# Performance work log

Hardware: AMD Instinct MI355X
Metric: run time of the kernel (lower is better)

The kernel has to match this reference:

```python
import jax, jax.numpy as jnp
from jax import lax
import numpy as np

B, N, C = 128, 196, 768
H = 8
HD = C // H  # 96
FF = 3       # focusing factor
KS = 5       # dwc kernel size


def setup_inputs() -> dict:
    key = jax.random.key(0)
    ks = jax.random.split(key, 12)
    std = 0.02
    inp = {
        'x': jax.random.normal(ks[0], (B, N, C), dtype=jnp.float32),
        'Wq': jax.random.normal(ks[1], (C, C), dtype=jnp.float32) * std,
        'bq': jnp.zeros((C,), dtype=jnp.float32),
        'Wk': jax.random.normal(ks[2], (C, C), dtype=jnp.float32) * std,
        'bk': jnp.zeros((C,), dtype=jnp.float32),
        'Wv': jax.random.normal(ks[3], (C, C), dtype=jnp.float32) * std,
        'bv': jnp.zeros((C,), dtype=jnp.float32),
        'pos_enc': jax.random.normal(ks[4], (1, N, C), dtype=jnp.float32) * std,
        'scale_param': jnp.zeros((1, 1, C), dtype=jnp.float32),
        'dwc_w': jax.random.normal(ks[5], (HD, 1, KS, KS), dtype=jnp.float32) * np.sqrt(2.0 / (KS * KS)),
        'dwc_b': jnp.zeros((HD,), dtype=jnp.float32),
        'Wp': jax.random.normal(ks[6], (C, C), dtype=jnp.float32) * std,
        'bp': jnp.zeros((C,), dtype=jnp.float32),
    }
    return inp


def _focused_attn(x, Wq, bq, Wk, bk, Wv, bv, pos_enc, scale_param, dwc_w, dwc_b, Wp, bp):
    b, n, c = x.shape
    q = x @ Wq + bq
    k = x @ Wk + bk
    v = x @ Wv + bv
    k = k + pos_enc

    scale = jax.nn.softplus(scale_param)
    q = (jax.nn.relu(q) + 1e-6) / scale
    k = (jax.nn.relu(k) + 1e-6) / scale
    # focusing: raise to power FF, restore original L2 norm (over full channel dim)
    q_norm = jnp.linalg.norm(q, axis=-1, keepdims=True)
    k_norm = jnp.linalg.norm(k, axis=-1, keepdims=True)
    q = q ** FF
    k = k ** FF
    q = q / jnp.linalg.norm(q, axis=-1, keepdims=True) * q_norm
    k = k / jnp.linalg.norm(k, axis=-1, keepdims=True) * k_norm

    # (b, n, H*hd) -> (b*H, n, hd)
    def split_heads(t):
        return t.reshape(b, n, H, HD).transpose(0, 2, 1, 3).reshape(b * H, n, HD)

    q, k, v = split_heads(q), split_heads(k), split_heads(v)

    i = j = n
    cdim = ddim = HD
    z = 1.0 / (jnp.einsum('bic,bc->bi', q, k.sum(axis=1)) + 1e-6)
    if i * j * (cdim + ddim) > cdim * ddim * (i + j):
        kv = jnp.einsum('bjc,bjd->bcd', k, v)              # (b*H, hd, hd)
        out = jnp.einsum('bic,bcd,bi->bid', q, kv, z)
    else:
        qk = jnp.einsum('bic,bjc->bij', q, k)
        out = jnp.einsum('bij,bjd,bi->bid', qk, v, z)

    # depthwise conv feature map on v reshaped to sqrt(n) x sqrt(n)
    num = int(round(n ** 0.5))
    fm = v.transpose(0, 2, 1).reshape(b * H, HD, num, num)
    fm = lax.conv_general_dilated(
        fm, dwc_w, window_strides=(1, 1), padding='SAME',
        feature_group_count=HD,
        dimension_numbers=('NCHW', 'OIHW', 'NCHW'))
    fm = fm + dwc_b[None, :, None, None]
    fm = fm.reshape(b * H, HD, n).transpose(0, 2, 1)

    out = out + fm
    out = out.reshape(b, H, n, HD).transpose(0, 2, 1, 3).reshape(b, n, c)
    return out @ Wp + bp


def reference(x, Wq, bq, Wk, bk, Wv, bv, pos_enc, scale_param, dwc_w, dwc_b, Wp, bp):
    return _focused_attn(x, Wq, bq, Wk, bk, Wv, bv, pos_enc, scale_param, dwc_w, dwc_b, Wp, bp)
```

## Files before the change

### kernel.cpp

```cpp
#include <hip/hip_runtime.h>
#include <hip/hip_bf16.h>
#include <math.h>


#define MROWS 25088
#define CDIM 768
#define HDIM 96
#define NTOK 196
#define BHN 1024
#define K2 1536

typedef __attribute__((ext_vector_type(8))) short bf16x8;
typedef __attribute__((ext_vector_type(4))) float f32x4;

__device__ __forceinline__ short f2bf(float x) {
  unsigned u = __float_as_uint(x);
  unsigned r = (u + 0x7fffu + ((u >> 16) & 1u)) >> 16;
  return (short)r;
}
__device__ __forceinline__ float bf2f(short s) {
  return __uint_as_float(((unsigned)(unsigned short)s) << 16);
}

__device__ __forceinline__ void gload16(const short* g, short* l) {
  __builtin_amdgcn_global_load_lds(
      (const __attribute__((address_space(1))) void*)g,
      (__attribute__((address_space(3))) void*)l, 16, 0, 0);
}

__device__ __forceinline__ unsigned cvt2(float x, float y, float& rx, float& ry) {
  __hip_bfloat162 hb = __float22bfloat162_rn(make_float2(x, y));
  float2 hf = __bfloat1622float2(hb);
  rx = x - hf.x; ry = y - hf.y;
  unsigned u;
  __builtin_memcpy(&u, &hb, 4);
  return u;
}
__device__ __forceinline__ unsigned cvt2n(float x, float y) {
  __hip_bfloat162 hb = __float22bfloat162_rn(make_float2(x, y));
  unsigned u;
  __builtin_memcpy(&u, &hb, 4);
  return u;
}

__global__ __launch_bounds__(256) void split_wt(const float* __restrict__ W0,
                                                const float* __restrict__ W1,
                                                const float* __restrict__ W2,
                                                const float* __restrict__ W3,
                                                short* __restrict__ outbase) {
  const float* W;
  switch (blockIdx.z) {
    case 0: W = W0; break;
    case 1: W = W1; break;
    case 2: W = W2; break;
    default: W = W3; break;
  }
  short* O = outbase + (size_t)blockIdx.z * 768 * K2;
  __shared__ float t[32][33];
  const int n0 = blockIdx.x * 32, k0 = blockIdx.y * 32;
  const int tx = threadIdx.x & 31, ty = threadIdx.x >> 5;
#pragma unroll
  for (int i = 0; i < 32; i += 8) t[ty + i][tx] = W[(size_t)(k0 + ty + i) * 768 + n0 + tx];
  __syncthreads();
#pragma unroll
  for (int i = 0; i < 32; i += 8) {
    float v = t[tx][ty + i];
    short h = f2bf(v), l = f2bf(v - bf2f(h));
    O[(size_t)(n0 + ty + i) * K2 + k0 + tx] = h;
    O[(size_t)(n0 + ty + i) * K2 + 768 + k0 + tx] = l;
  }
}

__device__ __forceinline__ void gemm_mfma_body(const float* __restrict__ A,
                                               const short* __restrict__ Bt2,
                                               const float* __restrict__ bias,
                                               const float* __restrict__ pos,
                                               float* __restrict__ C, bool addPos) {
  __shared__ short Ah[128 * 32];
  __shared__ short Al[128 * 32];
  __shared__ short Bh[128 * 32];
  __shared__ short Bl[128 * 32];
  const int tid = threadIdx.x;
  const int lane = tid & 63;
  const int w = tid >> 6, wr = w >> 1, wc = w & 1;

  const int hw = blockIdx.x + 6 * blockIdx.y;
  const int tile = (hw & 7) * 147 + (hw >> 3);
  const int bx = tile % 6, by = tile / 6;
  const int row0 = by * 128, col0 = bx * 128;

  const int ar = tid >> 1;
  const int ah_ = tid & 1;
  const int am = (tid >> 2) & 3;
  const int s0 = (2 * ah_) ^ am, s1 = (2 * ah_ + 1) ^ am;
  const float* gA = A + (size_t)(row0 + ar) * CDIM + ah_ * 16;
  short* lAh0 = Ah + ar * 32 + s0 * 8;
  short* lAh1 = Ah + ar * 32 + s1 * 8;
  short* lAl0 = Al + ar * 32 + s0 * 8;
  short* lAl1 = Al + ar * 32 + s1 * 8;

  const int brow = w * 32 + (lane >> 2);
  const int bslot = (lane & 3) ^ ((lane >> 3) & 3);
  const short* gBh = Bt2 + (size_t)(col0 + brow) * K2 + bslot * 8;
  const short* gBl = gBh + 768;
  short* ldsBh0 = Bh + (w * 32) * 32;
  short* ldsBh1 = Bh + (w * 32 + 16) * 32;
  short* ldsBl0 = Bl + (w * 32) * 32;
  short* ldsBl1 = Bl + (w * 32 + 16) * 32;

  f32x4 acc[4][4];
#pragma unroll
  for (int i = 0; i < 4; i++)
#pragma unroll
    for (int j = 0; j < 4; j++) acc[i][j] = (f32x4){0.f, 0.f, 0.f, 0.f};

  const int fr = lane & 15;
  const int k16 = lane >> 4;
  const int rslot = k16 ^ ((fr >> 1) & 3);
  const int rofs = fr * 32 + rslot * 8;

#pragma unroll 1
  for (int k0 = 0; k0 < CDIM; k0 += 32) {
    float4 a0 = *(const float4*)(gA + k0);
    float4 a1 = *(const float4*)(gA + k0 + 4);
    float4 a2 = *(const float4*)(gA + k0 + 8);
    float4 a3 = *(const float4*)(gA + k0 + 12);
    float r[16];
    unsigned h0 = cvt2(a0.x, a0.y, r[0], r[1]);
    unsigned h1 = cvt2(a0.z, a0.w, r[2], r[3]);
    unsigned h2 = cvt2(a1.x, a1.y, r[4], r[5]);
    unsigned h3 = cvt2(a1.z, a1.w, r[6], r[7]);
    unsigned h4 = cvt2(a2.x, a2.y, r[8], r[9]);
    unsigned h5 = cvt2(a2.z, a2.w, r[10], r[11]);
    unsigned h6 = cvt2(a3.x, a3.y, r[12], r[13]);
    unsigned h7 = cvt2(a3.z, a3.w, r[14], r[15]);
    unsigned l0 = cvt2n(r[0], r[1]),  l1 = cvt2n(r[2], r[3]);
    unsigned l2 = cvt2n(r[4], r[5]),  l3 = cvt2n(r[6], r[7]);
    unsigned l4 = cvt2n(r[8], r[9]),  l5 = cvt2n(r[10], r[11]);
    unsigned l6 = cvt2n(r[12], r[13]), l7 = cvt2n(r[14], r[15]);

    __syncthreads();
    gload16(gBh + k0, ldsBh0);
    gload16(gBh + 16 * K2 + k0, ldsBh1);
    gload16(gBl + k0, ldsBl0);
    gload16(gBl + 16 * K2 + k0, ldsBl1);
    *(uint4*)lAh0 = make_uint4(h0, h1, h2, h3);
    *(uint4*)lAh1 = make_uint4(h4, h5, h6, h7);
    *(uint4*)lAl0 = make_uint4(l0, l1, l2, l3);
    *(uint4*)lAl1 = make_uint4(l4, l5, l6, l7);
    __syncthreads();

    bf16x8 fah[4], fal[4], fbh[4], fbl[4];
#pragma unroll
    for (int i = 0; i < 4; i++) {
      const int arr = (wr * 64 + i * 16) * 32 + rofs;
      const int brr = (wc * 64 + i * 16) * 32 + rofs;
      fah[i] = *(const bf16x8*)&Ah[arr];
      fal[i] = *(const bf16x8*)&Al[arr];
      fbh[i] = *(const bf16x8*)&Bh[brr];
      fbl[i] = *(const bf16x8*)&Bl[brr];
    }
#pragma unroll
    for (int i = 0; i < 4; i++)
#pragma unroll
      for (int j = 0; j < 4; j++)
        acc[i][j] = __builtin_amdgcn_mfma_f32_16x16x32_bf16(fah[i], fbh[j], acc[i][j], 0, 0, 0);
#pragma unroll
    for (int i = 0; i < 4; i++)
#pragma unroll
      for (int j = 0; j < 4; j++)
        acc[i][j] = __builtin_amdgcn_mfma_f32_16x16x32_bf16(fah[i], fbl[j], acc[i][j], 0, 0, 0);
#pragma unroll
    for (int i = 0; i < 4; i++)
#pragma unroll
      for (int j = 0; j < 4; j++)
        acc[i][j] = __builtin_amdgcn_mfma_f32_16x16x32_bf16(fal[i], fbh[j], acc[i][j], 0, 0, 0);
  }

  const int rg = (lane >> 4) * 4;
#pragma unroll
  for (int i = 0; i < 4; i++) {
#pragma unroll
    for (int j = 0; j < 4; j++) {
      f32x4 v = acc[i][j];
      const int gcol = col0 + wc * 64 + j * 16 + fr;
      const float bb = bias[gcol];
#pragma unroll
      for (int r2 = 0; r2 < 4; r2++) {
        const int grow = row0 + wr * 64 + i * 16 + rg + r2;
        float val = v[r2] + bb;
        if (addPos) val += pos[(grow % NTOK) * CDIM + gcol];
        C[(size_t)grow * CDIM + gcol] = val;
      }
    }
  }
}

__global__ __launch_bounds__(256) void mfma_qkv(const float* __restrict__ x,
    const short* __restrict__ wt2,
    const float* __restrict__ b0, const float* __restrict__ b1, const float* __restrict__ b2,
    const float* __restrict__ pos,
    float* __restrict__ o0, float* __restrict__ o1, float* __restrict__ o2) {
  const short* Bt; const float* bias; float* C; bool addPos = false;
  switch (blockIdx.z) {
    case 0: Bt = wt2;                         bias = b0; C = o0; break;
    case 1: Bt = wt2 + (size_t)768 * K2;      bias = b1; C = o1; addPos = true; break;
    default: Bt = wt2 + (size_t)2 * 768 * K2; bias = b2; C = o2; break;
  }
  gemm_mfma_body(x, Bt, bias, pos, C, addPos);
}

__global__ __launch_bounds__(256) void mfma_proj(const float* __restrict__ y,
    const short* __restrict__ wt2p, const float* __restrict__ bias,
    float* __restrict__ C) {
  gemm_mfma_body(y, wt2p, bias, nullptr, C, false);
}

__device__ __forceinline__ void wave_reduce2(float& a, float& b) {
#pragma unroll
  for (int off = 32; off > 0; off >>= 1) {
    a += __shfl_xor(a, off, 64);
    b += __shfl_xor(b, off, 64);
  }
}

__global__ __launch_bounds__(256) void focus_kernel(float* __restrict__ q,
                                                    float* __restrict__ k,
                                                    const float* __restrict__ sp) {
  const int row = blockIdx.x * 4 + (threadIdx.x >> 6);
  const int lane = threadIdx.x & 63;
  float* qb = q + (size_t)row * CDIM;
  float* kb = k + (size_t)row * CDIM;

  float tq[12], tk[12];
  float sq = 0.f, sk = 0.f;
#pragma unroll
  for (int s = 0; s < 3; s++) {
    const int c = s * 256 + lane * 4;
    float4 qv = *(const float4*)&qb[c];
    float4 kv4 = *(const float4*)&kb[c];
    float4 spv = *(const float4*)&sp[c];
#pragma unroll
    for (int j = 0; j < 4; j++) {
      float scp = j == 0 ? spv.x : j == 1 ? spv.y : j == 2 ? spv.z : spv.w;
      float qq  = j == 0 ? qv.x  : j == 1 ? qv.y  : j == 2 ? qv.z  : qv.w;
      float kk  = j == 0 ? kv4.x : j == 1 ? kv4.y : j == 2 ? kv4.z : kv4.w;
      float scale = fmaxf(scp, 0.f) + log1pf(expf(-fabsf(scp)));
      float inv = 1.f / scale;
      float aq = (fmaxf(qq, 0.f) + 1e-6f) * inv;
      float ak = (fmaxf(kk, 0.f) + 1e-6f) * inv;
      tq[s * 4 + j] = aq; tk[s * 4 + j] = ak;
      sq += aq * aq; sk += ak * ak;
    }
  }
  wave_reduce2(sq, sk);
  const float nq1 = sqrtf(sq), nk1 = sqrtf(sk);

  float s2q = 0.f, s2k = 0.f;
#pragma unroll
  for (int j = 0; j < 12; j++) {
    float cq = tq[j] * tq[j] * tq[j];
    float ck = tk[j] * tk[j] * tk[j];
    s2q += cq * cq; s2k += ck * ck;
  }
  wave_reduce2(s2q, s2k);
  const float rq = nq1 / sqrtf(s2q);
  const float rk = nk1 / sqrtf(s2k);

#pragma unroll
  for (int s = 0; s < 3; s++) {
    const int c = s * 256 + lane * 4;
    float4 oq, ok;
#pragma unroll
    for (int j = 0; j < 4; j++) {
      float a = tq[s * 4 + j], b = tk[s * 4 + j];
      float vq = a * a * a * rq, vk = b * b * b * rk;
      if (j == 0) { oq.x = vq; ok.x = vk; }
      else if (j == 1) { oq.y = vq; ok.y = vk; }
      else if (j == 2) { oq.z = vq; ok.z = vk; }
      else { oq.w = vq; ok.w = vk; }
    }
    *(float4*)&qb[c] = oq;
    *(float4*)&kb[c] = ok;
  }
}

__global__ __launch_bounds__(128) void ksum_kernel(const float* __restrict__ k,
                                                   float* __restrict__ ksum) {
  const int bh = blockIdx.x;
  const int b = bh >> 3, h = bh & 7;
  const int d = threadIdx.x;
  if (d >= HDIM) return;
  const float* base = k + (size_t)(b * NTOK) * CDIM + h * HDIM + d;
  float s = 0.f;
  for (int j = 0; j < NTOK; ++j) s += base[(size_t)j * CDIM];
  ksum[bh * HDIM + d] = s;
}

__global__ __launch_bounds__(256) void kv_kernel(const float* __restrict__ k,
                                                 const float* __restrict__ v,
                                                 float* __restrict__ kv) {
  const int bh = blockIdx.x;
  const int b = bh >> 3, h = bh & 7;
  const size_t base = (size_t)(b * NTOK) * CDIM + h * HDIM;
  __shared__ float ks[28][96];
  __shared__ float vs[28][96];
  const int tid = threadIdx.x;
  const int tx = tid & 15, ty = tid >> 4;
  float acc[6][6];
#pragma unroll
  for (int i = 0; i < 6; i++)
#pragma unroll
    for (int j = 0; j < 6; j++) acc[i][j] = 0.f;

  for (int j0 = 0; j0 < NTOK; j0 += 28) {
    for (int idx = tid; idx < 28 * 96; idx += 256) {
      int jr = idx / 96, d = idx % 96;
      size_t g = base + (size_t)(j0 + jr) * CDIM + d;
      ks[jr][d] = k[g];
      vs[jr][d] = v[g];
    }
    __syncthreads();
#pragma unroll 4
    for (int j = 0; j < 28; ++j) {
      float a[6], bb[6];
#pragma unroll
      for (int i = 0; i < 6; i++) a[i] = ks[j][ty * 6 + i];
#pragma unroll
      for (int i = 0; i < 6; i++) bb[i] = vs[j][tx * 6 + i];
#pragma unroll
      for (int i = 0; i < 6; i++)
#pragma unroll
        for (int jj = 0; jj < 6; jj++) acc[i][jj] += a[i] * bb[jj];
    }
    __syncthreads();
  }
#pragma unroll
  for (int i = 0; i < 6; i++)
#pragma unroll
    for (int j = 0; j < 6; j++)
      kv[(size_t)bh * (HDIM * HDIM) + (ty * 6 + i) * HDIM + tx * 6 + j] = acc[i][j];
}

__global__ __launch_bounds__(256) void attn_out_kernel(const float* __restrict__ q,
                                                       const float* __restrict__ kvmat,
                                                       const float* __restrict__ ksum,
                                                       float* __restrict__ y) {
  const int bh = blockIdx.x;
  const int b = bh >> 3, h = bh & 7;
  const size_t base = (size_t)(b * NTOK) * CDIM + h * HDIM;
  __shared__ float kvs[HDIM * HDIM];
  __shared__ float qs[64][97];
  __shared__ float ksum_s[HDIM];
  const int tid = threadIdx.x;
  const int tx = tid & 15, ty = tid >> 4;
  const int d0 = tx * 6;

  for (int idx = tid; idx < HDIM * HDIM; idx += 256) kvs[idx] = kvmat[(size_t)bh * (HDIM * HDIM) + idx];
  if (tid < HDIM) ksum_s[tid] = ksum[bh * HDIM + tid];

  for (int i0 = 0; i0 < NTOK; i0 += 64) {
    int nrows = NTOK - i0; if (nrows > 64) nrows = 64;
    __syncthreads();
    for (int idx = tid; idx < nrows * 96; idx += 256) {
      int rr = idx / 96, d = idx % 96;
      qs[rr][d] = q[base + (size_t)(i0 + rr) * CDIM + d];
    }
    __syncthreads();

    float zz[4];
#pragma unroll
    for (int rr = 0; rr < 4; rr++) {
      int r2 = ty * 4 + rr;
      float part = 0.f;
#pragma unroll
      for (int i = 0; i < 6; i++) part += qs[r2][d0 + i] * ksum_s[d0 + i];
#pragma unroll
      for (int m = 8; m >= 1; m >>= 1) part += __shfl_xor(part, m, 16);
      zz[rr] = 1.f / (part + 1e-6f);
    }

    float acc[4][6];
#pragma unroll
    for (int rr = 0; rr < 4; rr++)
#pragma unroll
      for (int i = 0; i < 6; i++) acc[rr][i] = 0.f;

    for (int c = 0; c < HDIM; ++c) {
      float kvv[6];
#pragma unroll
      for (int i = 0; i < 6; i++) kvv[i] = kvs[c * HDIM + d0 + i];
#pragma unroll
      for (int rr = 0; rr < 4; rr++) {
        float qv = qs[ty * 4 + rr][c];
#pragma unroll
        for (int i = 0; i < 6; i++) acc[rr][i] += qv * kvv[i];
      }
    }
#pragma unroll
    for (int rr = 0; rr < 4; rr++) {
      int r2 = i0 + ty * 4 + rr;
      if (r2 < NTOK) {
#pragma unroll
        for (int i = 0; i < 6; i++) y[base + (size_t)r2 * CDIM + d0 + i] = acc[rr][i] * zz[rr];
      }
    }
  }
}

__global__ __launch_bounds__(256) void dwconv_kernel(const float* __restrict__ v,
                                                     const float* __restrict__ w,
                                                     const float* __restrict__ bias,
                                                     float* __restrict__ y) {
  const int bh = blockIdx.x;
  const int b = bh >> 3, h = bh & 7;
  const int ch0 = blockIdx.y * 32;
  const size_t base = (size_t)(b * NTOK) * CDIM + h * HDIM + ch0;
  __shared__ float vs[NTOK][32];
  __shared__ float ws_s[32][25];
  const int tid = threadIdx.x;

  for (int idx = tid; idx < NTOK * 32; idx += 256) {
    int j = idx >> 5, ch = idx & 31;
    vs[j][ch] = v[base + (size_t)j * CDIM + ch];
  }
  for (int idx = tid; idx < 32 * 25; idx += 256) {
    int ch = idx / 25, kk = idx % 25;
    ws_s[ch][kk] = w[(ch0 + ch) * 25 + kk];
  }
  __syncthreads();

  const int ch = tid & 31, pg = tid >> 5;
  const float bval = bias[ch0 + ch];
  for (int p = pg; p < NTOK; p += 8) {
    int r2 = p / 14, cl = p % 14;
    float acc = 0.f;
#pragma unroll
    for (int dr = 0; dr < 5; dr++) {
      int rr = r2 + dr - 2;
      if (rr < 0 || rr >= 14) continue;
#pragma unroll
      for (int dc = 0; dc < 5; dc++) {
        int cc = cl + dc - 2;
        if (cc < 0 || cc >= 14) continue;
        acc += vs[rr * 14 + cc][ch] * ws_s[ch][dr * 5 + dc];
      }
    }
    y[base + (size_t)p * CDIM + ch] += acc + bval;
  }
}

extern "C" void kernel_launch(void* const* d_in, const int* in_sizes, int n_in,
                              void* d_out, int out_size, void* d_ws, size_t ws_size,
                              hipStream_t stream) {
  const float* x    = (const float*)d_in[0];
  const float* Wq   = (const float*)d_in[1];
  const float* bq   = (const float*)d_in[2];
  const float* Wk   = (const float*)d_in[3];
  const float* bk   = (const float*)d_in[4];
  const float* Wv   = (const float*)d_in[5];
  const float* bv   = (const float*)d_in[6];
  const float* pos  = (const float*)d_in[7];
  const float* sp   = (const float*)d_in[8];
  const float* dwcw = (const float*)d_in[9];
  const float* dwcb = (const float*)d_in[10];
  const float* Wp   = (const float*)d_in[11];
  const float* bp   = (const float*)d_in[12];
  float* out = (float*)d_out;

  const size_t MC = (size_t)MROWS * CDIM;
  char* ws = (char*)d_ws;
  float* k    = (float*)(ws);
  float* v    = (float*)(ws + MC * 4);
  short* wt2  = (short*)(ws + 2 * MC * 4);
  float* kv   = (float*)(ws + 2 * MC * 4 + (size_t)4 * 768 * K2 * 2);
  float* ksum = kv + (size_t)BHN * HDIM * HDIM;
  float* q = out;
  float* y = k;

  split_wt<<<dim3(24, 24, 4), 256, 0, stream>>>(Wq, Wk, Wv, Wp, wt2);
  mfma_qkv<<<dim3(6, 196, 3), 256, 0, stream>>>(x, wt2, bq, bk, bv, pos, q, k, v);
  focus_kernel<<<MROWS / 4, 256, 0, stream>>>(q, k, sp);
  ksum_kernel<<<BHN, 128, 0, stream>>>(k, ksum);
  kv_kernel<<<BHN, 256, 0, stream>>>(k, v, kv);
  attn_out_kernel<<<BHN, 256, 0, stream>>>(q, kv, ksum, y);
  dwconv_kernel<<<dim3(BHN, 3), 256, 0, stream>>>(v, dwcw, dwcb, y);
  mfma_proj<<<dim3(6, 196, 1), 256, 0, stream>>>(y, wt2 + (size_t)3 * 768 * K2, bp, out);
}
```

Measured before the change: 937.6 us.

## Pre-split activations into bf16 hi/lo and load GEMM A tiles via direct LDS

Adds a split_act kernel that converts x into bf16 hi/lo pairs once, and has dwconv write the projection input y directly in split form. Both GEMMs then load A and B with global_load_lds instead of converting fp32 A inside the k-loop. ksum is folded into kv_kernel, and some LDS reads are vectorized. This trades extra global write/read passes for the split activations against removing the repeated per-block conversion work and register pressure in the GEMM loops.

```diff
diff --git a/kernel.cpp b/kernel.cpp
--- a/kernel.cpp
+++ b/kernel.cpp
@@ -26,21 +26,6 @@
   __builtin_amdgcn_global_load_lds(
       (const __attribute__((address_space(1))) void*)g,
       (__attribute__((address_space(3))) void*)l, 16, 0, 0);
-}
-
-__device__ __forceinline__ unsigned cvt2(float x, float y, float& rx, float& ry) {
-  __hip_bfloat162 hb = __float22bfloat162_rn(make_float2(x, y));
-  float2 hf = __bfloat1622float2(hb);
-  rx = x - hf.x; ry = y - hf.y;
-  unsigned u;
-  __builtin_memcpy(&u, &hb, 4);
-  return u;
-}
-__device__ __forceinline__ unsigned cvt2n(float x, float y) {
-  __hip_bfloat162 hb = __float22bfloat162_rn(make_float2(x, y));
-  unsigned u;
-  __builtin_memcpy(&u, &hb, 4);
-  return u;
 }
 
 __global__ __launch_bounds__(256) void split_wt(const float* __restrict__ W0,
@@ -71,11 +56,26 @@
   }
 }
 
-__device__ __forceinline__ void gemm_mfma_body(const float* __restrict__ A,
-                                               const short* __restrict__ Bt2,
-                                               const float* __restrict__ bias,
-                                               const float* __restrict__ pos,
-                                               float* __restrict__ C, bool addPos) {
+__global__ __launch_bounds__(256) void split_act(const float* __restrict__ in,
+                                                 short* __restrict__ out2) {
+  int idx = blockIdx.x * 256 + threadIdx.x;
+  if (idx >= MROWS * 192) return;
+  int m = idx / 192, c4 = (idx % 192) * 4;
+  float4 v = *(const float4*)&in[(size_t)m * CDIM + c4];
+  short4 hi, lo;
+  hi.x = f2bf(v.x); lo.x = f2bf(v.x - bf2f(hi.x));
+  hi.y = f2bf(v.y); lo.y = f2bf(v.y - bf2f(hi.y));
+  hi.z = f2bf(v.z); lo.z = f2bf(v.z - bf2f(hi.z));
+  hi.w = f2bf(v.w); lo.w = f2bf(v.w - bf2f(hi.w));
+  *(short4*)&out2[(size_t)m * K2 + c4] = hi;
+  *(short4*)&out2[(size_t)m * K2 + 768 + c4] = lo;
+}
+
+__device__ __forceinline__ void gemm_mfma_body_pre(const short* __restrict__ A2,
+                                                   const short* __restrict__ Bt2,
+                                                   const float* __restrict__ bias,
+                                                   const float* __restrict__ pos,
+                                                   float* __restrict__ C, bool addPos) {
   __shared__ short Ah[128 * 32];
   __shared__ short Al[128 * 32];
   __shared__ short Bh[128 * 32];
@@ -89,24 +89,18 @@
   const int bx = tile % 6, by = tile / 6;
   const int row0 = by * 128, col0 = bx * 128;
 
-  const int ar = tid >> 1;
-  const int ah_ = tid & 1;
-  const int am = (tid >> 2) & 3;
-  const int s0 = (2 * ah_) ^ am, s1 = (2 * ah_ + 1) ^ am;
-  const float* gA = A + (size_t)(row0 + ar) * CDIM + ah_ * 16;
-  short* lAh0 = Ah + ar * 32 + s0 * 8;
-  short* lAh1 = Ah + ar * 32 + s1 * 8;
-  short* lAl0 = Al + ar * 32 + s0 * 8;
-  short* lAl1 = Al + ar * 32 + s1 * 8;
-
-  const int brow = w * 32 + (lane >> 2);
-  const int bslot = (lane & 3) ^ ((lane >> 3) & 3);
-  const short* gBh = Bt2 + (size_t)(col0 + brow) * K2 + bslot * 8;
-  const short* gBl = gBh + 768;
-  short* ldsBh0 = Bh + (w * 32) * 32;
-  short* ldsBh1 = Bh + (w * 32 + 16) * 32;
-  short* ldsBl0 = Bl + (w * 32) * 32;
-  short* ldsBl1 = Bl + (w * 32 + 16) * 32;
+  const int srow = w * 32 + (lane >> 2);
+  const int slot = (lane & 3) ^ ((lane >> 3) & 3);
+  const short* gA = A2 + (size_t)(row0 + srow) * K2 + slot * 8;
+  const short* gB = Bt2 + (size_t)(col0 + srow) * K2 + slot * 8;
+  short* dA0 = Ah + (w * 32) * 32;
+  short* dA1 = Ah + (w * 32 + 16) * 32;
+  short* dAl0 = Al + (w * 32) * 32;
+  short* dAl1 = Al + (w * 32 + 16) * 32;
+  short* dB0 = Bh + (w * 32) * 32;
+  short* dB1 = Bh + (w * 32 + 16) * 32;
+  short* dBl0 = Bl + (w * 32) * 32;
+  short* dBl1 = Bl + (w * 32 + 16) * 32;
 
   f32x4 acc[4][4];
 #pragma unroll
@@ -121,33 +115,15 @@
 
 #pragma unroll 1
   for (int k0 = 0; k0 < CDIM; k0 += 32) {
-    float4 a0 = *(const float4*)(gA + k0);
-    float4 a1 = *(const float4*)(gA + k0 + 4);
-    float4 a2 = *(const float4*)(gA + k0 + 8);
-    float4 a3 = *(const float4*)(gA + k0 + 12);
-    float r[16];
-    unsigned h0 = cvt2(a0.x, a0.y, r[0], r[1]);
-    unsigned h1 = cvt2(a0.z, a0.w, r[2], r[3]);
-    unsigned h2 = cvt2(a1.x, a1.y, r[4], r[5]);
-    unsigned h3 = cvt2(a1.z, a1.w, r[6], r[7]);
-    unsigned h4 = cvt2(a2.x, a2.y, r[8], r[9]);
-    unsigned h5 = cvt2(a2.z, a2.w, r[10], r[11]);
-    unsigned h6 = cvt2(a3.x, a3.y, r[12], r[13]);
-    unsigned h7 = cvt2(a3.z, a3.w, r[14], r[15]);
-    unsigned l0 = cvt2n(r[0], r[1]),  l1 = cvt2n(r[2], r[3]);
-    unsigned l2 = cvt2n(r[4], r[5]),  l3 = cvt2n(r[6], r[7]);
-    unsigned l4 = cvt2n(r[8], r[9]),  l5 = cvt2n(r[10], r[11]);
-    unsigned l6 = cvt2n(r[12], r[13]), l7 = cvt2n(r[14], r[15]);
-
-    __syncthreads();
-    gload16(gBh + k0, ldsBh0);
-    gload16(gBh + 16 * K2 + k0, ldsBh1);
-    gload16(gBl + k0, ldsBl0);
-    gload16(gBl + 16 * K2 + k0, ldsBl1);
-    *(uint4*)lAh0 = make_uint4(h0, h1, h2, h3);
-    *(uint4*)lAh1 = make_uint4(h4, h5, h6, h7);
-    *(uint4*)lAl0 = make_uint4(l0, l1, l2, l3);
-    *(uint4*)lAl1 = make_uint4(l4, l5, l6, l7);
+    __syncthreads();
+    gload16(gA + k0, dA0);
+    gload16(gA + 16 * K2 + k0, dA1);
+    gload16(gA + 768 + k0, dAl0);
+    gload16(gA + 768 + 16 * K2 + k0, dAl1);
+    gload16(gB + k0, dB0);
+    gload16(gB + 16 * K2 + k0, dB1);
+    gload16(gB + 768 + k0, dBl0);
+    gload16(gB + 768 + 16 * K2 + k0, dBl1);
     __syncthreads();
 
     bf16x8 fah[4], fal[4], fbh[4], fbl[4];
@@ -196,7 +172,7 @@
   }
 }
 
-__global__ __launch_bounds__(256) void mfma_qkv(const float* __restrict__ x,
+__global__ __launch_bounds__(256) void mfma_qkv_pre(const short* __restrict__ x2,
     const short* __restrict__ wt2,
     const float* __restrict__ b0, const float* __restrict__ b1, const float* __restrict__ b2,
     const float* __restrict__ pos,
@@ -207,13 +183,13 @@
     case 1: Bt = wt2 + (size_t)768 * K2;      bias = b1; C = o1; addPos = true; break;
     default: Bt = wt2 + (size_t)2 * 768 * K2; bias = b2; C = o2; break;
   }
-  gemm_mfma_body(x, Bt, bias, pos, C, addPos);
-}
-
-__global__ __launch_bounds__(256) void mfma_proj(const float* __restrict__ y,
+  gemm_mfma_body_pre(x2, Bt, bias, pos, C, addPos);
+}
+
+__global__ __launch_bounds__(256) void mfma_proj_pre(const short* __restrict__ y2,
     const short* __restrict__ wt2p, const float* __restrict__ bias,
     float* __restrict__ C) {
-  gemm_mfma_body(y, wt2p, bias, nullptr, C, false);
+  gemm_mfma_body_pre(y2, wt2p, bias, nullptr, C, false);
 }
 
 __device__ __forceinline__ void wave_reduce2(float& a, float& b) {
@@ -285,21 +261,10 @@
   }
 }
 
-__global__ __launch_bounds__(128) void ksum_kernel(const float* __restrict__ k,
-                                                   float* __restrict__ ksum) {
-  const int bh = blockIdx.x;
-  const int b = bh >> 3, h = bh & 7;
-  const int d = threadIdx.x;
-  if (d >= HDIM) return;
-  const float* base = k + (size_t)(b * NTOK) * CDIM + h * HDIM + d;
-  float s = 0.f;
-  for (int j = 0; j < NTOK; ++j) s += base[(size_t)j * CDIM];
-  ksum[bh * HDIM + d] = s;
-}
-
 __global__ __launch_bounds__(256) void kv_kernel(const float* __restrict__ k,
                                                  const float* __restrict__ v,
-                                                 float* __restrict__ kv) {
+                                                 float* __restrict__ kv,
+                                                 float* __restrict__ ksum) {
   const int bh = blockIdx.x;
   const int b = bh >> 3, h = bh & 7;
   const size_t base = (size_t)(b * NTOK) * CDIM + h * HDIM;
@@ -312,6 +277,7 @@
   for (int i = 0; i < 6; i++)
 #pragma unroll
     for (int j = 0; j < 6; j++) acc[i][j] = 0.f;
+  float kcol = 0.f;
 
   for (int j0 = 0; j0 < NTOK; j0 += 28) {
     for (int idx = tid; idx < 28 * 96; idx += 256) {
@@ -321,13 +287,17 @@
       vs[jr][d] = v[g];
     }
     __syncthreads();
+    if (tid < 96) {
+#pragma unroll
+      for (int jr = 0; jr < 28; ++jr) kcol += ks[jr][tid];
+    }
 #pragma unroll 4
     for (int j = 0; j < 28; ++j) {
       float a[6], bb[6];
 #pragma unroll
-      for (int i = 0; i < 6; i++) a[i] = ks[j][ty * 6 + i];
-#pragma unroll
-      for (int i = 0; i < 6; i++) bb[i] = vs[j][tx * 6 + i];
+      for (int i = 0; i < 3; i++) *(float2*)&a[i * 2]  = *(const float2*)&ks[j][ty * 6 + i * 2];
+#pragma unroll
+      for (int i = 0; i < 3; i++) *(float2*)&bb[i * 2] = *(const float2*)&vs[j][tx * 6 + i * 2];
 #pragma unroll
       for (int i = 0; i < 6; i++)
 #pragma unroll
@@ -340,6 +310,7 @@
 #pragma unroll
     for (int j = 0; j < 6; j++)
       kv[(size_t)bh * (HDIM * HDIM) + (ty * 6 + i) * HDIM + tx * 6 + j] = acc[i][j];
+  if (tid < 96) ksum[bh * HDIM + tid] = kcol;
 }
 
 __global__ __launch_bounds__(256) void attn_out_kernel(const float* __restrict__ q,
@@ -389,7 +360,7 @@
     for (int c = 0; c < HDIM; ++c) {
       float kvv[6];
 #pragma unroll
-      for (int i = 0; i < 6; i++) kvv[i] = kvs[c * HDIM + d0 + i];
+      for (int i = 0; i < 3; i++) *(float2*)&kvv[i * 2] = *(const float2*)&kvs[c * HDIM + d0 + i * 2];
 #pragma unroll
       for (int rr = 0; rr < 4; rr++) {
         float qv = qs[ty * 4 + rr][c];
@@ -411,11 +382,13 @@
 __global__ __launch_bounds__(256) void dwconv_kernel(const float* __restrict__ v,
                                                      const float* __restrict__ w,
                                                      const float* __restrict__ bias,
-                                                     float* __restrict__ y) {
+                                                     const float* __restrict__ y,
+                                                     short* __restrict__ y2) {
   const int bh = blockIdx.x;
   const int b = bh >> 3, h = bh & 7;
   const int ch0 = blockIdx.y * 32;
   const size_t base = (size_t)(b * NTOK) * CDIM + h * HDIM + ch0;
+  const size_t col = h * HDIM + ch0;
   __shared__ float vs[NTOK][32];
   __shared__ float ws_s[32][25];
   const int tid = threadIdx.x;
@@ -446,7 +419,12 @@
         acc += vs[rr * 14 + cc][ch] * ws_s[ch][dr * 5 + dc];
       }
     }
-    y[base + (size_t)p * CDIM + ch] += acc + bval;
+    float val = y[base + (size_t)p * CDIM + ch] + acc + bval;
+    short hh = f2bf(val);
+    short ll = f2bf(val - bf2f(hh));
+    const size_t row = (size_t)(b * NTOK + p);
+    y2[row * K2 + col + ch] = hh;
+    y2[row * K2 + 768 + col + ch] = ll;
   }
 }
 
@@ -469,21 +447,25 @@
   float* out = (float*)d_out;
 
   const size_t MC = (size_t)MROWS * CDIM;
+  const size_t WT2B = (size_t)4 * 768 * K2 * 2;
   char* ws = (char*)d_ws;
   float* k    = (float*)(ws);
   float* v    = (float*)(ws + MC * 4);
   short* wt2  = (short*)(ws + 2 * MC * 4);
-  float* kv   = (float*)(ws + 2 * MC * 4 + (size_t)4 * 768 * K2 * 2);
-  float* ksum = kv + (size_t)BHN * HDIM * HDIM;
+  char* R3 = ws + 2 * MC * 4 + WT2B;
+  short* x2   = (short*)R3;
+  float* kv   = (float*)R3;
+  float* ksum = (float*)(R3 + (size_t)BHN * HDIM * HDIM * 4);
+  short* y2   = (short*)R3;
   float* q = out;
   float* y = k;
 
   split_wt<<<dim3(24, 24, 4), 256, 0, stream>>>(Wq, Wk, Wv, Wp, wt2);
-  mfma_qkv<<<dim3(6, 196, 3), 256, 0, stream>>>(x, wt2, bq, bk, bv, pos, q, k, v);
+  split_act<<<(MROWS * 192 + 255) / 256, 256, 0, stream>>>(x, x2);
+  mfma_qkv_pre<<<dim3(6, 196, 3), 256, 0, stream>>>(x2, wt2, bq, bk, bv, pos, q, k, v);
   focus_kernel<<<MROWS / 4, 256, 0, stream>>>(q, k, sp);
-  ksum_kernel<<<BHN, 128, 0, stream>>>(k, ksum);
-  kv_kernel<<<BHN, 256, 0, stream>>>(k, v, kv);
+  kv_kernel<<<BHN, 256, 0, stream>>>(k, v, kv, ksum);
   attn_out_kernel<<<BHN, 256, 0, stream>>>(q, kv, ksum, y);
-  dwconv_kernel<<<dim3(BHN, 3), 256, 0, stream>>>(v, dwcw, dwcb, y);
-  mfma_proj<<<dim3(6, 196, 1), 256, 0, stream>>>(y, wt2 + (size_t)3 * 768 * K2, bp, out);
-}
+  dwconv_kernel<<<dim3(BHN, 3), 256, 0, stream>>>(v, dwcw, dwcb, y, y2);
+  mfma_proj_pre<<<dim3(6, 196, 1), 256, 0, stream>>>(y2, wt2 + (size_t)3 * 768 * K2, bp, out);
+}
```

Result: no change. 931.8 us (-0.6%).
